# Performance work log

Measured on AMD Instinct MI355X. Metric: run time of the kernel, lower is better.

## Reference

```python
import jax, jax.numpy as jnp
import numpy as np

B, N, D, C = 256, 2000, 512, 100


def setup_inputs() -> dict:
    key = jax.random.key(0)
    k1, k2, k3, k4 = jax.random.split(key, 4)
    inputs = jax.random.normal(k1, (B, D), dtype=jnp.float32)
    support_tensors = jax.random.normal(k2, (N, D), dtype=jnp.float32)
    label_idx = jax.random.randint(k3, (N,), 0, C)
    support_labels = jax.nn.one_hot(label_idx, C, dtype=jnp.float32)
    kernel_w = jax.random.normal(k4, (D,), dtype=jnp.float32) * 0.05
    kernel_b = jnp.zeros((), dtype=jnp.float32)
    return {
        "inputs": inputs,
        "support_tensors": support_tensors,
        "support_labels": support_labels,
        "kernel_w": kernel_w,
        "kernel_b": kernel_b,
    }


def reference(inputs, support_tensors, support_labels, kernel_w, kernel_b):
    # Pairwise Cartesian product (batch x support): |a - b|, shape [B, N, D]
    diff = jnp.abs(inputs[:, None, :] - support_tensors[None, :, :])
    # Siamese kernel: sigmoid(Dense(1)(|a-b|)) -> scores [B, N]
    pair_wise_scores = jax.nn.sigmoid(jnp.einsum("bnd,d->bn", diff, kernel_w) + kernel_b)
    # Per-class aggregation: matmul with one-hot labels, then mean per class
    class_sums = pair_wise_scores @ support_labels  # [B, C]
    class_counts = jnp.sum(support_labels, axis=0)  # [C]
    # tf.math.divide_no_nan semantics
    return jnp.where(class_counts != 0, class_sums / class_counts, 0.0)
```

## Files before the change

kernel.cpp:

```cpp
#include <hip/hip_runtime.h>

#define B_SZ 256
#define N_SZ 2000
#define N_PAD 2048
#define D_SZ 512
#define C_SZ 100
#define BT 4
#define JW 4
#define ZSPLIT 16
#define D4 (D_SZ / 4)
#define DC8 (D_SZ / 8)

typedef __fp16 h2 __attribute__((ext_vector_type(2)));

struct alignas(16) H8 { h2 x, y, z, w; };
struct alignas(8)  H4 { h2 lo, hi; };

static __device__ __forceinline__ h2 habs2(h2 v) {
    unsigned u = __builtin_bit_cast(unsigned, v) & 0x7FFF7FFFu;
    return __builtin_bit_cast(h2, u);
}

#if __has_builtin(__builtin_amdgcn_fdot2)
static __device__ __forceinline__ float DOT2(h2 d, h2 wv, float c) {
    return __builtin_amdgcn_fdot2(d, wv, c, false);
}
#else
static __device__ __forceinline__ float DOT2(h2 d, h2 wv, float c) {
    return c + (float)d.x * (float)wv.x + (float)d.y * (float)wv.y;
}
#endif

__global__ void setup_kernel(const float* __restrict__ labels,
                             const float* __restrict__ inputs,
                             const float* __restrict__ w,
                             int* __restrict__ idx,
                             H4* __restrict__ inpH4,
                             __fp16* __restrict__ wH) {
    int bid = blockIdx.x, tid = threadIdx.x;
    if (bid < 8) {
        int n = bid * 256 + tid;
        if (n < N_SZ) {
            const float4* row = (const float4*)(labels + (size_t)n * C_SZ);
            int c = 0;
#pragma unroll
            for (int j = 0; j < C_SZ / 4; ++j) {
                float4 v = row[j];
                if (v.x > 0.5f) c = 4 * j + 0;
                if (v.y > 0.5f) c = 4 * j + 1;
                if (v.z > 0.5f) c = 4 * j + 2;
                if (v.w > 0.5f) c = 4 * j + 3;
            }
            idx[n] = c;
        }
    } else if (bid == 8) {
        wH[tid]       = (__fp16)w[tid];
        wH[tid + 256] = (__fp16)w[tid + 256];
    } else {
        int i4 = (bid - 9) * 256 + tid;
        float4 v = ((const float4*)inputs)[i4];
        H4 o;
        o.lo = __builtin_amdgcn_cvt_pkrtz(v.x, v.y);
        o.hi = __builtin_amdgcn_cvt_pkrtz(v.z, v.w);
        inpH4[i4] = o;
    }
}

__global__ void transposeH_kernel(const float4* __restrict__ sup4,
                                  H8* __restrict__ supH) {
    int t = blockIdx.x * 256 + threadIdx.x;
    int dc8 = t >> 11;
    int n   = t & (N_PAD - 1);
    H8 o = {};
    if (n < N_SZ) {
        float4 p = sup4[(size_t)n * D4 + 2 * dc8];
        float4 q = sup4[(size_t)n * D4 + 2 * dc8 + 1];
        o.x = __builtin_amdgcn_cvt_pkrtz(p.x, p.y);
        o.y = __builtin_amdgcn_cvt_pkrtz(p.z, p.w);
        o.z = __builtin_amdgcn_cvt_pkrtz(q.x, q.y);
        o.w = __builtin_amdgcn_cvt_pkrtz(q.z, q.w);
    }
    supH[t] = o;
}

__global__ __launch_bounds__(256, 3) void score_kernel(
    const H8* __restrict__ inpH8,
    const H8* __restrict__ supH,
    const H8* __restrict__ wH8,
    float* __restrict__ S)
{
    int tid = threadIdx.x;
    int b0  = blockIdx.x * BT;
    int dc0 = blockIdx.y * JW;

    unsigned vz = 0;
    asm volatile("" : "+v"(vz));

    H8 af[BT][JW];
    H8 wf[JW];
#pragma unroll
    for (int i = 0; i < BT; ++i) {
        const H8* ap = inpH8 + (size_t)(b0 + i) * DC8 + dc0 + vz;
#pragma unroll
        for (int j = 0; j < JW; ++j) af[i][j] = ap[j];
    }
    {
        const H8* wp = wH8 + dc0 + vz;
#pragma unroll
        for (int j = 0; j < JW; ++j) wf[j] = wp[j];
    }

    const H8* sp0 = supH + (size_t)(dc0 + 0) * N_PAD + tid;
    const H8* sp1 = supH + (size_t)(dc0 + 1) * N_PAD + tid;
    const H8* sp2 = supH + (size_t)(dc0 + 2) * N_PAD + tid;
    const H8* sp3 = supH + (size_t)(dc0 + 3) * N_PAD + tid;

    float* Sp0 = S + ((size_t)blockIdx.y * B_SZ + b0) * N_PAD + tid;

#define STEP(J, SV)                                                  \
    {                                                                \
        H8 wv = wf[J];                                               \
        _Pragma("unroll") for (int i = 0; i < BT; ++i) {             \
            H8 a = af[i][J];                                         \
            acc[i] = DOT2(habs2(a.x - SV.x), wv.x, acc[i]);          \
            acc[i] = DOT2(habs2(a.y - SV.y), wv.y, acc[i]);          \
            acc[i] = DOT2(habs2(a.z - SV.z), wv.z, acc[i]);          \
            acc[i] = DOT2(habs2(a.w - SV.w), wv.w, acc[i]);          \
        }                                                            \
    }

    H8 sv0 = sp0[0], sv1 = sp1[0], sv2 = sp2[0], sv3 = sp3[0];

#pragma unroll 1
    for (int n0 = 0; n0 < N_PAD - 256; n0 += 256) {
        float acc[BT] = {0.f, 0.f, 0.f, 0.f};
        H8 nx0 = sp0[n0 + 256];
        STEP(0, sv0);
        H8 nx1 = sp1[n0 + 256];
        STEP(1, sv1);
        H8 nx2 = sp2[n0 + 256];
        STEP(2, sv2);
        H8 nx3 = sp3[n0 + 256];
        STEP(3, sv3);
#pragma unroll
        for (int i = 0; i < BT; ++i)
            Sp0[(size_t)i * N_PAD + n0] = acc[i];
        sv0 = nx0; sv1 = nx1; sv2 = nx2; sv3 = nx3;
    }
    {
        float acc[BT] = {0.f, 0.f, 0.f, 0.f};
        STEP(0, sv0); STEP(1, sv1); STEP(2, sv2); STEP(3, sv3);
#pragma unroll
        for (int i = 0; i < BT; ++i)
            Sp0[(size_t)i * N_PAD + (N_PAD - 256)] = acc[i];
    }
#undef STEP
}

__global__ void agg_kernel(const float* __restrict__ S,
                           const int* __restrict__ idx,
                           const float* __restrict__ bias_p,
                           float* __restrict__ out) {
    __shared__ float sums[C_SZ];
    __shared__ float cnts[C_SZ];
    int b = blockIdx.x;
    int t = threadIdx.x;
    if (t < C_SZ) { sums[t] = 0.f; cnts[t] = 0.f; }
    __syncthreads();
    float bias = *bias_p;
    for (int n = t; n < N_SZ; n += 512) {
        float logit = bias;
#pragma unroll
        for (int z = 0; z < ZSPLIT; ++z)
            logit += S[((size_t)z * B_SZ + b) * N_PAD + n];
        float s = 1.0f / (1.0f + __expf(-logit));
        int c = idx[n];
        atomicAdd(&sums[c], s);
        atomicAdd(&cnts[c], 1.0f);
    }
    __syncthreads();
    if (t < C_SZ) {
        float cnt = cnts[t];
        out[(size_t)b * C_SZ + t] = (cnt != 0.f) ? sums[t] / cnt : 0.f;
    }
}

extern "C" void kernel_launch(void* const* d_in, const int* in_sizes, int n_in,
                              void* d_out, int out_size, void* d_ws, size_t ws_size,
                              hipStream_t stream) {
    const float* inputs  = (const float*)d_in[0];
    const float* support = (const float*)d_in[1];
    const float* labels  = (const float*)d_in[2];
    const float* w       = (const float*)d_in[3];
    const float* bias    = (const float*)d_in[4];
    float* out = (float*)d_out;

    int*     idx  = (int*)d_ws;
    __fp16*  wH   = (__fp16*)((char*)d_ws + 8192);
    __fp16*  inpH = (__fp16*)((char*)d_ws + 16384);
    H8*      supH = (H8*)((char*)d_ws + 524288);
    float*   S    = (float*)((char*)d_ws + 4 * 1024 * 1024);

    setup_kernel<<<dim3(9 + B_SZ * D_SZ / 4 / 256), dim3(256), 0, stream>>>(
        labels, inputs, w, idx, (H4*)inpH, wH);

    transposeH_kernel<<<dim3(DC8 * N_PAD / 256), dim3(256), 0, stream>>>(
        (const float4*)support, supH);

    dim3 grid(B_SZ / BT, ZSPLIT);
    score_kernel<<<grid, dim3(256), 0, stream>>>(
        (const H8*)inpH, supH, (const H8*)wH, S);

    agg_kernel<<<dim3(B_SZ), dim3(512), 0, stream>>>(S, idx, bias, out);
}
```

Before: 42.07 us.

## Split score kernel over N tiles with D halves to shrink partial-sum traffic

Reorganizes the score kernel so each block covers 128 support rows and half of the feature dimension, looping over D in-register, instead of 16 D-slices each sweeping all of N. This cuts the partial-score buffer from 16 slices to 2, which reduces global write traffic and the reads in the aggregation kernel, now launched with 256 threads. In exchange, each thread now reloads inputs and weights from memory (likely cache) inside the D loop instead of holding them in registers, and the grid becomes much larger with smaller blocks.

```diff
diff --git a/kernel.cpp b/kernel.cpp
--- a/kernel.cpp
+++ b/kernel.cpp
@@ -6,10 +6,10 @@
 #define D_SZ 512
 #define C_SZ 100
 #define BT 4
-#define JW 4
-#define ZSPLIT 16
+#define NT 128
 #define D4 (D_SZ / 4)
 #define DC8 (D_SZ / 8)
+#define DHALF (DC8 / 2)
 
 typedef __fp16 h2 __attribute__((ext_vector_type(2)));
 
@@ -83,81 +83,73 @@
     supH[t] = o;
 }
 
-__global__ __launch_bounds__(256, 3) void score_kernel(
+__global__ __launch_bounds__(NT, 4) void score_kernel(
     const H8* __restrict__ inpH8,
     const H8* __restrict__ supH,
     const H8* __restrict__ wH8,
-    float* __restrict__ S)
+    float* __restrict__ S2)
 {
     int tid = threadIdx.x;
+    int n   = blockIdx.y * NT + tid;
     int b0  = blockIdx.x * BT;
-    int dc0 = blockIdx.y * JW;
+    int dz  = blockIdx.z;
+    int dcb = dz * DHALF;
 
     unsigned vz = 0;
     asm volatile("" : "+v"(vz));
 
-    H8 af[BT][JW];
-    H8 wf[JW];
+    const H8* __restrict__ a0 = inpH8 + (size_t)(b0 + 0) * DC8 + dcb + vz;
+    const H8* __restrict__ a1 = inpH8 + (size_t)(b0 + 1) * DC8 + dcb + vz;
+    const H8* __restrict__ a2 = inpH8 + (size_t)(b0 + 2) * DC8 + dcb + vz;
+    const H8* __restrict__ a3 = inpH8 + (size_t)(b0 + 3) * DC8 + dcb + vz;
+    const H8* __restrict__ wp = wH8 + dcb + vz;
+    const H8* __restrict__ sp = supH + (size_t)dcb * N_PAD + n;
+
+    float acc[BT] = {0.f, 0.f, 0.f, 0.f};
+
+#define ROW(AP, I, DC, SV, WV)                                       \
+    {                                                                \
+        H8 a = AP[DC];                                               \
+        acc[I] = DOT2(habs2(a.x - SV.x), WV.x, acc[I]);              \
+        acc[I] = DOT2(habs2(a.y - SV.y), WV.y, acc[I]);              \
+        acc[I] = DOT2(habs2(a.z - SV.z), WV.z, acc[I]);              \
+        acc[I] = DOT2(habs2(a.w - SV.w), WV.w, acc[I]);              \
+    }
+
+#define PAIR(DC, S0, S1)                                             \
+    {                                                                \
+        H8 w0 = wp[DC], w1 = wp[(DC) + 1];                           \
+        ROW(a0, 0, (DC), S0, w0)                                     \
+        ROW(a1, 1, (DC), S0, w0)                                     \
+        ROW(a2, 2, (DC), S0, w0)                                     \
+        ROW(a3, 3, (DC), S0, w0)                                     \
+        ROW(a0, 0, (DC) + 1, S1, w1)                                 \
+        ROW(a1, 1, (DC) + 1, S1, w1)                                 \
+        ROW(a2, 2, (DC) + 1, S1, w1)                                 \
+        ROW(a3, 3, (DC) + 1, S1, w1)                                 \
+    }
+
+    H8 s0 = sp[0];
+    H8 s1 = sp[(size_t)1 * N_PAD];
+
+#pragma unroll 1
+    for (int dc = 0; dc < DHALF - 2; dc += 2) {
+        H8 p0 = sp[(size_t)(dc + 2) * N_PAD];
+        H8 p1 = sp[(size_t)(dc + 3) * N_PAD];
+        PAIR(dc, s0, s1);
+        s0 = p0; s1 = p1;
+    }
+    PAIR(DHALF - 2, s0, s1);
+#undef PAIR
+#undef ROW
+
+    float* __restrict__ Sp = S2 + ((size_t)dz * B_SZ + b0) * N_PAD + n;
 #pragma unroll
-    for (int i = 0; i < BT; ++i) {
-        const H8* ap = inpH8 + (size_t)(b0 + i) * DC8 + dc0 + vz;
-#pragma unroll
-        for (int j = 0; j < JW; ++j) af[i][j] = ap[j];
-    }
-    {
-        const H8* wp = wH8 + dc0 + vz;
-#pragma unroll
-        for (int j = 0; j < JW; ++j) wf[j] = wp[j];
-    }
-
-    const H8* sp0 = supH + (size_t)(dc0 + 0) * N_PAD + tid;
-    const H8* sp1 = supH + (size_t)(dc0 + 1) * N_PAD + tid;
-    const H8* sp2 = supH + (size_t)(dc0 + 2) * N_PAD + tid;
-    const H8* sp3 = supH + (size_t)(dc0 + 3) * N_PAD + tid;
-
-    float* Sp0 = S + ((size_t)blockIdx.y * B_SZ + b0) * N_PAD + tid;
-
-#define STEP(J, SV)                                                  \
-    {                                                                \
-        H8 wv = wf[J];                                               \
-        _Pragma("unroll") for (int i = 0; i < BT; ++i) {             \
-            H8 a = af[i][J];                                         \
-            acc[i] = DOT2(habs2(a.x - SV.x), wv.x, acc[i]);          \
-            acc[i] = DOT2(habs2(a.y - SV.y), wv.y, acc[i]);          \
-            acc[i] = DOT2(habs2(a.z - SV.z), wv.z, acc[i]);          \
-            acc[i] = DOT2(habs2(a.w - SV.w), wv.w, acc[i]);          \
-        }                                                            \
-    }
-
-    H8 sv0 = sp0[0], sv1 = sp1[0], sv2 = sp2[0], sv3 = sp3[0];
-
-#pragma unroll 1
-    for (int n0 = 0; n0 < N_PAD - 256; n0 += 256) {
-        float acc[BT] = {0.f, 0.f, 0.f, 0.f};
-        H8 nx0 = sp0[n0 + 256];
-        STEP(0, sv0);
-        H8 nx1 = sp1[n0 + 256];
-        STEP(1, sv1);
-        H8 nx2 = sp2[n0 + 256];
-        STEP(2, sv2);
-        H8 nx3 = sp3[n0 + 256];
-        STEP(3, sv3);
-#pragma unroll
-        for (int i = 0; i < BT; ++i)
-            Sp0[(size_t)i * N_PAD + n0] = acc[i];
-        sv0 = nx0; sv1 = nx1; sv2 = nx2; sv3 = nx3;
-    }
-    {
-        float acc[BT] = {0.f, 0.f, 0.f, 0.f};
-        STEP(0, sv0); STEP(1, sv1); STEP(2, sv2); STEP(3, sv3);
-#pragma unroll
-        for (int i = 0; i < BT; ++i)
-            Sp0[(size_t)i * N_PAD + (N_PAD - 256)] = acc[i];
-    }
-#undef STEP
-}
-
-__global__ void agg_kernel(const float* __restrict__ S,
+    for (int i = 0; i < BT; ++i)
+        Sp[(size_t)i * N_PAD] = acc[i];
+}
+
+__global__ void agg_kernel(const float* __restrict__ S2,
                            const int* __restrict__ idx,
                            const float* __restrict__ bias_p,
                            float* __restrict__ out) {
@@ -168,11 +160,9 @@
     if (t < C_SZ) { sums[t] = 0.f; cnts[t] = 0.f; }
     __syncthreads();
     float bias = *bias_p;
-    for (int n = t; n < N_SZ; n += 512) {
-        float logit = bias;
-#pragma unroll
-        for (int z = 0; z < ZSPLIT; ++z)
-            logit += S[((size_t)z * B_SZ + b) * N_PAD + n];
+    for (int n = t; n < N_SZ; n += 256) {
+        float logit = bias + S2[(size_t)b * N_PAD + n]
+                           + S2[((size_t)B_SZ + b) * N_PAD + n];
         float s = 1.0f / (1.0f + __expf(-logit));
         int c = idx[n];
         atomicAdd(&sums[c], s);
@@ -199,7 +189,7 @@
     __fp16*  wH   = (__fp16*)((char*)d_ws + 8192);
     __fp16*  inpH = (__fp16*)((char*)d_ws + 16384);
     H8*      supH = (H8*)((char*)d_ws + 524288);
-    float*   S    = (float*)((char*)d_ws + 4 * 1024 * 1024);
+    float*   S2   = (float*)((char*)d_ws + 4 * 1024 * 1024);
 
     setup_kernel<<<dim3(9 + B_SZ * D_SZ / 4 / 256), dim3(256), 0, stream>>>(
         labels, inputs, w, idx, (H4*)inpH, wH);
@@ -207,9 +197,9 @@
     transposeH_kernel<<<dim3(DC8 * N_PAD / 256), dim3(256), 0, stream>>>(
         (const float4*)support, supH);
 
-    dim3 grid(B_SZ / BT, ZSPLIT);
-    score_kernel<<<grid, dim3(256), 0, stream>>>(
-        (const H8*)inpH, supH, (const H8*)wH, S);
-
-    agg_kernel<<<dim3(B_SZ), dim3(512), 0, stream>>>(S, idx, bias, out);
-}
+    dim3 grid(B_SZ / BT, N_PAD / NT, 2);
+    score_kernel<<<grid, dim3(NT), 0, stream>>>(
+        (const H8*)inpH, supH, (const H8*)wH, S2);
+
+    agg_kernel<<<dim3(B_SZ), dim3(256), 0, stream>>>(S2, idx, bias, out);
+}
```

Measured after the change: 45.62 us. 8.4% more time.

## Fuse support transpose into setup and reduce split-D partials via atomics

Applied to the files above, without the earlier changes.

Merges the support-tensor fp16 transpose into the setup kernel, with reads changed to be coalesced along D, which removes one kernel launch. The score kernel now accumulates its 16 split-D partials into a single B×N buffer with float atomicAdd instead of writing 16 separate slabs. The aggregation kernel then reads one value per pair instead of summing 16, at the cost of an extra memset, atomic contention and order-dependent float summation. The aggregation block size also drops to 256 threads.

```diff
diff --git a/kernel.cpp b/kernel.cpp
--- a/kernel.cpp
+++ b/kernel.cpp
@@ -34,12 +34,35 @@
 __global__ void setup_kernel(const float* __restrict__ labels,
                              const float* __restrict__ inputs,
                              const float* __restrict__ w,
+                             const float4* __restrict__ sup4,
                              int* __restrict__ idx,
                              H4* __restrict__ inpH4,
-                             __fp16* __restrict__ wH) {
+                             H4* __restrict__ wH4,
+                             H8* __restrict__ supH) {
     int bid = blockIdx.x, tid = threadIdx.x;
-    if (bid < 8) {
-        int n = bid * 256 + tid;
+    if (bid < 512) {
+        int t   = bid * 256 + tid;
+        int n   = t >> 6;
+        int dc8 = t & 63;
+        H8 o = {};
+        if (n < N_SZ) {
+            float4 p = sup4[(size_t)n * D4 + 2 * dc8];
+            float4 q = sup4[(size_t)n * D4 + 2 * dc8 + 1];
+            o.x = __builtin_amdgcn_cvt_pkrtz(p.x, p.y);
+            o.y = __builtin_amdgcn_cvt_pkrtz(p.z, p.w);
+            o.z = __builtin_amdgcn_cvt_pkrtz(q.x, q.y);
+            o.w = __builtin_amdgcn_cvt_pkrtz(q.z, q.w);
+        }
+        supH[(size_t)dc8 * N_PAD + n] = o;
+    } else if (bid < 640) {
+        int i4 = (bid - 512) * 256 + tid;
+        float4 v = ((const float4*)inputs)[i4];
+        H4 o;
+        o.lo = __builtin_amdgcn_cvt_pkrtz(v.x, v.y);
+        o.hi = __builtin_amdgcn_cvt_pkrtz(v.z, v.w);
+        inpH4[i4] = o;
+    } else if (bid < 648) {
+        int n = (bid - 640) * 256 + tid;
         if (n < N_SZ) {
             const float4* row = (const float4*)(labels + (size_t)n * C_SZ);
             int c = 0;
@@ -53,34 +76,15 @@
             }
             idx[n] = c;
         }
-    } else if (bid == 8) {
-        wH[tid]       = (__fp16)w[tid];
-        wH[tid + 256] = (__fp16)w[tid + 256];
     } else {
-        int i4 = (bid - 9) * 256 + tid;
-        float4 v = ((const float4*)inputs)[i4];
-        H4 o;
-        o.lo = __builtin_amdgcn_cvt_pkrtz(v.x, v.y);
-        o.hi = __builtin_amdgcn_cvt_pkrtz(v.z, v.w);
-        inpH4[i4] = o;
-    }
-}
-
-__global__ void transposeH_kernel(const float4* __restrict__ sup4,
-                                  H8* __restrict__ supH) {
-    int t = blockIdx.x * 256 + threadIdx.x;
-    int dc8 = t >> 11;
-    int n   = t & (N_PAD - 1);
-    H8 o = {};
-    if (n < N_SZ) {
-        float4 p = sup4[(size_t)n * D4 + 2 * dc8];
-        float4 q = sup4[(size_t)n * D4 + 2 * dc8 + 1];
-        o.x = __builtin_amdgcn_cvt_pkrtz(p.x, p.y);
-        o.y = __builtin_amdgcn_cvt_pkrtz(p.z, p.w);
-        o.z = __builtin_amdgcn_cvt_pkrtz(q.x, q.y);
-        o.w = __builtin_amdgcn_cvt_pkrtz(q.z, q.w);
-    }
-    supH[t] = o;
+        if (tid < D_SZ / 4) {
+            float4 v = ((const float4*)w)[tid];
+            H4 o;
+            o.lo = __builtin_amdgcn_cvt_pkrtz(v.x, v.y);
+            o.hi = __builtin_amdgcn_cvt_pkrtz(v.z, v.w);
+            wH4[tid] = o;
+        }
+    }
 }
 
 __global__ __launch_bounds__(256, 3) void score_kernel(
@@ -115,7 +119,7 @@
     const H8* sp2 = supH + (size_t)(dc0 + 2) * N_PAD + tid;
     const H8* sp3 = supH + (size_t)(dc0 + 3) * N_PAD + tid;
 
-    float* Sp0 = S + ((size_t)blockIdx.y * B_SZ + b0) * N_PAD + tid;
+    float* Sp0 = S + (size_t)b0 * N_PAD + tid;
 
 #define STEP(J, SV)                                                  \
     {                                                                \
@@ -144,7 +148,7 @@
         STEP(3, sv3);
 #pragma unroll
         for (int i = 0; i < BT; ++i)
-            Sp0[(size_t)i * N_PAD + n0] = acc[i];
+            atomicAdd(&Sp0[(size_t)i * N_PAD + n0], acc[i]);
         sv0 = nx0; sv1 = nx1; sv2 = nx2; sv3 = nx3;
     }
     {
@@ -152,7 +156,7 @@
         STEP(0, sv0); STEP(1, sv1); STEP(2, sv2); STEP(3, sv3);
 #pragma unroll
         for (int i = 0; i < BT; ++i)
-            Sp0[(size_t)i * N_PAD + (N_PAD - 256)] = acc[i];
+            atomicAdd(&Sp0[(size_t)i * N_PAD + (N_PAD - 256)], acc[i]);
     }
 #undef STEP
 }
@@ -168,11 +172,8 @@
     if (t < C_SZ) { sums[t] = 0.f; cnts[t] = 0.f; }
     __syncthreads();
     float bias = *bias_p;
-    for (int n = t; n < N_SZ; n += 512) {
-        float logit = bias;
-#pragma unroll
-        for (int z = 0; z < ZSPLIT; ++z)
-            logit += S[((size_t)z * B_SZ + b) * N_PAD + n];
+    for (int n = t; n < N_SZ; n += 256) {
+        float logit = bias + S[(size_t)b * N_PAD + n];
         float s = 1.0f / (1.0f + __expf(-logit));
         int c = idx[n];
         atomicAdd(&sums[c], s);
@@ -196,20 +197,19 @@
     float* out = (float*)d_out;
 
     int*     idx  = (int*)d_ws;
-    __fp16*  wH   = (__fp16*)((char*)d_ws + 8192);
-    __fp16*  inpH = (__fp16*)((char*)d_ws + 16384);
+    H4*      wH4  = (H4*)((char*)d_ws + 8192);
+    H4*      inpH = (H4*)((char*)d_ws + 16384);
     H8*      supH = (H8*)((char*)d_ws + 524288);
     float*   S    = (float*)((char*)d_ws + 4 * 1024 * 1024);
 
-    setup_kernel<<<dim3(9 + B_SZ * D_SZ / 4 / 256), dim3(256), 0, stream>>>(
-        labels, inputs, w, idx, (H4*)inpH, wH);
-
-    transposeH_kernel<<<dim3(DC8 * N_PAD / 256), dim3(256), 0, stream>>>(
-        (const float4*)support, supH);
+    hipMemsetAsync(S, 0, (size_t)B_SZ * N_PAD * sizeof(float), stream);
+
+    setup_kernel<<<dim3(649), dim3(256), 0, stream>>>(
+        labels, inputs, w, (const float4*)support, idx, inpH, wH4, supH);
 
     dim3 grid(B_SZ / BT, ZSPLIT);
     score_kernel<<<grid, dim3(256), 0, stream>>>(
-        (const H8*)inpH, supH, (const H8*)wH, S);
-
-    agg_kernel<<<dim3(B_SZ), dim3(512), 0, stream>>>(S, idx, bias, out);
-}
+        (const H8*)inpH, supH, (const H8*)wH4, S);
+
+    agg_kernel<<<dim3(B_SZ), dim3(256), 0, stream>>>(S, idx, bias, out);
+}
```

After: 50.77 us. +20.7%, slower.
